# Optimization experiments

Hardware: AMD Instinct MI355X
Metric: run time of the kernel (lower is better)

Reference implementation:

```python
import jax, jax.numpy as jnp
import numpy as np

N = 100000          # total atoms in batch
M = 12              # max_num_neighbors
A = 64              # num_atom_features
B = 41              # num_bond_features
EPS = 1e-5          # haiku BatchNorm default


def setup_inputs() -> dict:
    key = jax.random.key(0)
    ks = jax.random.split(key, 6)
    neighbor_indices = jax.random.randint(ks[0], (N, M), 0, N, dtype=jnp.int32)
    atom_features = jax.random.normal(ks[1], (N, A), dtype=jnp.float32)
    bond_features = jax.random.normal(ks[2], (N, M, B), dtype=jnp.float32)
    in_f = 2 * A + B
    stdv = 1.0 / np.sqrt(in_f)
    W = jax.random.uniform(ks[3], (in_f, 2 * A), minval=-stdv, maxval=stdv, dtype=jnp.float32)
    b = jax.random.uniform(ks[4], (2 * A,), minval=-stdv, maxval=stdv, dtype=jnp.float32)
    return {
        "neighbor_indices": neighbor_indices,
        "atom_features": atom_features,
        "bond_features": bond_features,
        "W": W,
        "b": b,
        "bn1_scale": jnp.ones((2 * A,), jnp.float32),
        "bn1_offset": jnp.zeros((2 * A,), jnp.float32),
        "bn2_scale": jnp.ones((A,), jnp.float32),
        "bn2_offset": jnp.zeros((A,), jnp.float32),
    }


def _batchnorm(x, scale, offset):
    # training-mode batch norm over leading axis
    mean = jnp.mean(x, axis=0)
    var = jnp.var(x, axis=0)
    return (x - mean) * jax.lax.rsqrt(var + EPS) * scale + offset


def reference(neighbor_indices, atom_features, bond_features, W, b,
              bn1_scale, bn1_offset, bn2_scale, bn2_offset):
    n, m = neighbor_indices.shape
    a = atom_features.shape[1]
    # gather neighbor atom features: (N, M, A)
    nbr_feats = atom_features[neighbor_indices]
    self_feats = jnp.broadcast_to(atom_features[:, None, :], (n, m, a))
    total = jnp.concatenate([self_feats, nbr_feats, bond_features], axis=2)  # (N, M, 2A+B)
    gated = total @ W + b                                                    # (N, M, 2A)
    gated = _batchnorm(gated.reshape(-1, 2 * a), bn1_scale, bn1_offset).reshape(n, m, 2 * a)
    nbr_filter, nbr_core = jnp.split(gated, 2, axis=2)
    summed = jnp.sum(jax.nn.sigmoid(nbr_filter) * jax.nn.softplus(nbr_core), axis=1)  # (N, A)
    summed = _batchnorm(summed, bn2_scale, bn2_offset)
    return jax.nn.softplus(atom_features + summed)
```

## Files before the change

kernel.cpp:

```cpp
#include <hip/hip_runtime.h>

#define NATOM 100000
#define MNBR  12
#define RTOT  1200000
#define KF    169
#define NT    25000
#define NBP   1024
#define EPS   1e-5f

typedef short  bf16x8 __attribute__((ext_vector_type(8)));
typedef float  f32x4  __attribute__((ext_vector_type(4)));
typedef unsigned short us8 __attribute__((ext_vector_type(8)));

static __device__ __forceinline__ unsigned short f2bf(float x) {
    unsigned int u = __builtin_bit_cast(unsigned int, x);
    u = u + 0x7FFFu + ((u >> 16) & 1u);
    return (unsigned short)(u >> 16);
}
static __device__ __forceinline__ float softplus_f(float x) {
    return fmaxf(x, 0.f) + __logf(1.f + __expf(-fabsf(x)));
}
__device__ __forceinline__ void gload16(const void* g, void* l) {
    __builtin_amdgcn_global_load_lds((const __attribute__((address_space(1))) void*)g,
                                     (__attribute__((address_space(3))) void*)l, 16, 0, 0);
}
#define FENCE() asm volatile("" ::: "memory")

__global__ __launch_bounds__(256) void k0conv(const float* __restrict__ bond,
                                              const float* __restrict__ atom,
                                              const float* __restrict__ W,
                                              unsigned short* __restrict__ bondbf,
                                              unsigned short* __restrict__ atombf,
                                              unsigned short* __restrict__ Wbf) {
    int b = blockIdx.x;
    if (b < 28125) {
        int j0 = (b * 256 + (int)threadIdx.x) * 8;
        int r  = j0 / 48;
        int q  = j0 - r * 48;
        us8 o;
        #pragma unroll
        for (int e = 0; e < 8; ++e) {
            int c = q + e;
            float v = (c < 41) ? bond[(size_t)r * 41 + c] : 0.f;
            o[e] = f2bf(v);
        }
        *(us8*)(bondbf + j0) = o;
    } else if (b < 31250) {
        int i8 = ((b - 28125) * 256 + (int)threadIdx.x) * 8;
        float4 v0 = *(const float4*)(atom + i8);
        float4 v1 = *(const float4*)(atom + i8 + 4);
        us8 o;
        o[0]=f2bf(v0.x); o[1]=f2bf(v0.y); o[2]=f2bf(v0.z); o[3]=f2bf(v0.w);
        o[4]=f2bf(v1.x); o[5]=f2bf(v1.y); o[6]=f2bf(v1.z); o[7]=f2bf(v1.w);
        *(us8*)(atombf + i8) = o;
    } else {
        int i = (b - 31250) * 256 + (int)threadIdx.x;
        if (i < 128 * 192) {
            int c = i / 192, k = i - c * 192;
            Wbf[i] = (k < KF) ? f2bf(W[k * 128 + c]) : (unsigned short)0;
        }
    }
}

__global__ __launch_bounds__(256) void k_stats(const float* __restrict__ part,
                                               const float* __restrict__ scale,
                                               const float* __restrict__ offset,
                                               float* __restrict__ stats,
                                               int ncols, float invR) {
    int c = blockIdx.x, t = threadIdx.x;
    const float* ps = part + (size_t)c * NBP;
    const float* pq = part + (size_t)(ncols + c) * NBP;
    float s = 0.f, q = 0.f;
    for (int i = t; i < NBP; i += 256) { s += ps[i]; q += pq[i]; }
    __shared__ float rs[256], rq[256];
    rs[t] = s; rq[t] = q;
    __syncthreads();
    for (int o = 128; o > 0; o >>= 1) {
        if (t < o) { rs[t] += rs[t + o]; rq[t] += rq[t + o]; }
        __syncthreads();
    }
    if (t == 0) {
        float mean = rs[0] * invR;
        float var  = rq[0] * invR - mean * mean;
        float g = scale[c] * rsqrtf(var + EPS);
        stats[c] = g;
        stats[ncols + c] = offset[c] - mean * g;
    }
}

template<int PASS>
__global__ __launch_bounds__(256, 4) void kpass(const int* __restrict__ idx,
                                                const unsigned short* __restrict__ atombf,
                                                const unsigned short* __restrict__ bondbf,
                                                const unsigned short* __restrict__ Wbf,
                                                const float* __restrict__ stats1,
                                                float* __restrict__ part,
                                                float* __restrict__ summed) {
    __shared__ unsigned short AB[2][8704];
    __shared__ float sm[256];

    const int tid = threadIdx.x;
    const int wv  = tid >> 6;
    const int ln  = tid & 63;
    const int l15 = ln & 15;
    const int kq  = ln >> 4;
    const int blk = blockIdx.x;
    const int cf  = wv * 16 + l15;

    bf16x8 wfr[2][6];
    #pragma unroll
    for (int h = 0; h < 2; ++h) {
        int col = cf + h * 64;
        #pragma unroll
        for (int kc = 0; kc < 6; ++kc)
            wfr[h][kc] = *(const bf16x8*)((const char*)Wbf + col * 384 + kc * 64 + kq * 16);
    }
    float gf=0.f, hf=0.f, gc=0.f, hc=0.f;
    if (PASS == 2) {
        gf = stats1[cf];       hf = stats1[128 + cf];
        gc = stats1[64 + cf];  hc = stats1[192 + cf];
        sm[tid] = 0.f;
    }
    float s0 = 0.f, q0 = 0.f, s1 = 0.f, q1 = 0.f;

    int idxreg[4];
    auto PREFIDX = [&](int t) {
        #pragma unroll
        for (int j = 0; j < 4; ++j) {
            int i = wv * 4 + j;
            if (i >= 6 && i < 12) {
                int o = (i - 6) * 1024 + ln * 16;
                idxreg[j] = idx[t * 48 + (o >> 7)];
            }
        }
    };
    auto STAGE = [&](int t, int bsel) {
        unsigned short* buf = &AB[bsel][0];
        #pragma unroll
        for (int j = 0; j < 4; ++j) {
            int i = wv * 4 + j;
            if (i < 6) {
                int o  = i * 1024 + ln * 16;
                int os = o ^ (((o >> 7) & 7) << 4);
                int row = o >> 7;
                int n = (t * 48 + row) / 12;
                gload16(atombf + n * 64 + ((os & 127) >> 1), buf + (o >> 1));
            } else if (i < 12) {
                int o  = (i - 6) * 1024 + ln * 16;
                int os = o ^ (((o >> 7) & 7) << 4);
                int n = idxreg[j];
                gload16(atombf + n * 64 + ((os & 127) >> 1), buf + 3072 + (o >> 1));
            } else {
                int o = (i - 12) * 1024 + ln * 16;
                gload16(bondbf + (size_t)t * 2304 + (o >> 1), buf + 6144 + (o >> 1));
            }
        }
        if (wv == 0) {
            int o = 4 * 1024 + ln * 16;
            gload16(bondbf + (size_t)t * 2304 + (o >> 1), buf + 6144 + (o >> 1));
        }
    };

    int t0 = blk;
    PREFIDX(t0);
    asm volatile("s_waitcnt vmcnt(0)" ::: "memory");
    STAGE(t0, 0);
    if (t0 + NBP < NT) PREFIDX(t0 + NBP);

    int b = 0;
    for (int t = t0; t < NT; t += NBP) {
        bool hn = (t + NBP) < NT;
        if (PASS == 2) asm volatile("s_waitcnt lgkmcnt(0)" ::: "memory");
        __builtin_amdgcn_s_barrier();
        FENCE();
        if (hn) STAGE(t + NBP, b ^ 1);
        if (hn) {
            if (wv == 0) asm volatile("s_waitcnt vmcnt(5)" ::: "memory");
            else         asm volatile("s_waitcnt vmcnt(4)" ::: "memory");
        } else {
            asm volatile("s_waitcnt vmcnt(0)" ::: "memory");
        }
        __builtin_amdgcn_s_barrier();
        FENCE();

        const unsigned short* buf = &AB[b][0];
        f32x4 z = {0.f, 0.f, 0.f, 0.f};
        f32x4 acc[2][3];
        #pragma unroll
        for (int s = 0; s < 3; ++s) { acc[0][s] = z; acc[1][s] = z; }

        #pragma unroll
        for (int sub = 0; sub < 3; ++sub) {
            int row = sub * 16 + l15;
            #pragma unroll
            for (int kc = 0; kc < 6; ++kc) {
                const char* p;
                if (kc < 2)
                    p = (const char*)buf + ((row * 128 + kc * 64 + kq * 16) ^ ((row & 7) << 4));
                else if (kc < 4)
                    p = (const char*)(buf + 3072) + ((row * 128 + (kc - 2) * 64 + kq * 16) ^ ((row & 7) << 4));
                else
                    p = (const char*)(buf + 6144) + (row * 96 + (kc - 4) * 64 + kq * 16);
                bf16x8 a = *(const bf16x8*)p;
                acc[0][sub] = __builtin_amdgcn_mfma_f32_16x16x32_bf16(a, wfr[0][kc], acc[0][sub], 0, 0, 0);
                acc[1][sub] = __builtin_amdgcn_mfma_f32_16x16x32_bf16(a, wfr[1][kc], acc[1][sub], 0, 0, 0);
            }
        }

        if (PASS == 1) {
            #pragma unroll
            for (int sub = 0; sub < 3; ++sub)
                #pragma unroll
                for (int rg = 0; rg < 4; ++rg) {
                    float v0 = acc[0][sub][rg]; s0 += v0; q0 = fmaf(v0, v0, q0);
                    float v1 = acc[1][sub][rg]; s1 += v1; q1 = fmaf(v1, v1, q1);
                }
        } else {
            #pragma unroll
            for (int sub = 0; sub < 3; ++sub) {
                float ps = 0.f;
                #pragma unroll
                for (int rg = 0; rg < 4; ++rg) {
                    float yf = fmaf(acc[0][sub][rg], gf, hf);
                    float yc = fmaf(acc[1][sub][rg], gc, hc);
                    float sig = __builtin_amdgcn_rcpf(1.f + __expf(-yf));
                    ps = fmaf(sig, softplus_f(yc), ps);
                }
                int a = (sub * 16 + kq * 4) / 12;
                atomicAdd(&sm[a * 64 + cf], ps);
            }
            asm volatile("s_waitcnt lgkmcnt(0)" ::: "memory");
            __builtin_amdgcn_s_barrier();
            FENCE();
            float v = sm[tid];
            sm[tid] = 0.f;
            summed[(size_t)t * 256 + tid] = v;
            s0 += v; q0 = fmaf(v, v, q0);
        }
        b ^= 1;
        if (t + 2 * NBP < NT) PREFIDX(t + 2 * NBP);
    }

    if (PASS == 1) {
        s0 += __shfl_xor(s0, 16); s0 += __shfl_xor(s0, 32);
        q0 += __shfl_xor(q0, 16); q0 += __shfl_xor(q0, 32);
        s1 += __shfl_xor(s1, 16); s1 += __shfl_xor(s1, 32);
        q1 += __shfl_xor(q1, 16); q1 += __shfl_xor(q1, 32);
        if (ln < 16) {
            part[(size_t)cf * NBP + blk]          = s0;
            part[(size_t)(128 + cf) * NBP + blk]  = q0;
            part[(size_t)(64 + cf) * NBP + blk]   = s1;
            part[(size_t)(192 + cf) * NBP + blk]  = q1;
        }
    } else {
        __syncthreads();
        float* fs = (float*)&AB[0][0];
        fs[tid] = s0; fs[256 + tid] = q0;
        __syncthreads();
        if (tid < 64) {
            float S = fs[tid] + fs[tid + 64] + fs[tid + 128] + fs[tid + 192];
            float Q = fs[256 + tid] + fs[256 + tid + 64] + fs[256 + tid + 128] + fs[256 + tid + 192];
            part[(size_t)tid * NBP + blk]        = S;
            part[(size_t)(64 + tid) * NBP + blk] = Q;
        }
    }
}

__global__ __launch_bounds__(256) void k5_out(const float* __restrict__ atom,
                                              const float* __restrict__ summed,
                                              const float* __restrict__ stats2,
                                              float* __restrict__ out) {
    int i4 = blockIdx.x * 256 + threadIdx.x;
    int base = i4 * 4;
    int c = base & 63;
    float4 av = *(const float4*)(atom + base);
    float4 sv = *(const float4*)(summed + base);
    float4 ov;
    ov.x = softplus_f(av.x + stats2[c + 0] * sv.x + stats2[64 + c + 0]);
    ov.y = softplus_f(av.y + stats2[c + 1] * sv.y + stats2[64 + c + 1]);
    ov.z = softplus_f(av.z + stats2[c + 2] * sv.z + stats2[64 + c + 2]);
    ov.w = softplus_f(av.w + stats2[c + 3] * sv.w + stats2[64 + c + 3]);
    *(float4*)(out + base) = ov;
}

extern "C" void kernel_launch(void* const* d_in, const int* in_sizes, int n_in,
                              void* d_out, int out_size, void* d_ws, size_t ws_size,
                              hipStream_t stream) {
    const int*   idx  = (const int*)  d_in[0];
    const float* atom = (const float*)d_in[1];
    const float* bond = (const float*)d_in[2];
    const float* W    = (const float*)d_in[3];
    const float* bn1s = (const float*)d_in[5];
    const float* bn1o = (const float*)d_in[6];
    const float* bn2s = (const float*)d_in[7];
    const float* bn2o = (const float*)d_in[8];
    float* out = (float*)d_out;

    char* ws = (char*)d_ws;
    size_t off = 0;
    unsigned short* atombf = (unsigned short*)(ws + off); off += 12800000;
    unsigned short* bondbf = (unsigned short*)(ws + off); off += 115201024;
    unsigned short* Wbf    = (unsigned short*)(ws + off); off += 49152;
    float* part1  = (float*)(ws + off); off += 256 * NBP * 4;
    float* stats1 = (float*)(ws + off); off += 1024;
    float* part2  = (float*)(ws + off); off += 128 * NBP * 4;
    float* stats2 = (float*)(ws + off); off += 512;
    float* summed = (float*)(ws + off); off += 25600000;

    k0conv <<<31346, 256, 0, stream>>>(bond, atom, W, bondbf, atombf, Wbf);
    kpass<1><<<NBP, 256, 0, stream>>>(idx, atombf, bondbf, Wbf, stats1, part1, summed);
    k_stats<<<128, 256, 0, stream>>>(part1, bn1s, bn1o, stats1, 128, 1.f / (float)RTOT);
    kpass<2><<<NBP, 256, 0, stream>>>(idx, atombf, bondbf, Wbf, stats1, part2, summed);
    k_stats<<<64, 256, 0, stream>>>(part2, bn2s, bn2o, stats2, 64, 1.f / (float)NATOM);
    k5_out <<<6250, 256, 0, stream>>>(atom, summed, stats2, out);
}
```

Measured before the change: 584.7 us.

## Precompute self-atom projection and restructure passes into 512-thread blocks

Adds a kernel that computes each atom's self-feature contribution (atom @ W_self) once per atom rather than once per neighbor row. The main passes then drop the self K-chunks from the MFMA loop and add the staged precomputed value instead. Blocks double to 512 threads covering 96 rows per tile. Neighbor indices are now prefetched through LDS via global_load_lds, and the bond conversion kernel is rewritten to stage through shared memory for coalesced reads. This cuts MFMA work by about a third, at the cost of an extra N×128 fp32 buffer that must be written and then re-read in both passes, and a simpler single-stage wait (vmcnt(0)) that may reduce overlap.

```diff
diff --git a/kernel.cpp b/kernel.cpp
--- a/kernel.cpp
+++ b/kernel.cpp
@@ -4,9 +4,12 @@
 #define MNBR  12
 #define RTOT  1200000
 #define KF    169
-#define NT    25000
-#define NBP   1024
+#define NT    12500
+#define NBP   512
+#define IDXB  4800000
 #define EPS   1e-5f
+
+#define LBSZ  26752
 
 typedef short  bf16x8 __attribute__((ext_vector_type(8)));
 typedef float  f32x4  __attribute__((ext_vector_type(4)));
@@ -33,20 +36,25 @@
                                               unsigned short* __restrict__ atombf,
                                               unsigned short* __restrict__ Wbf) {
     int b = blockIdx.x;
-    if (b < 28125) {
-        int j0 = (b * 256 + (int)threadIdx.x) * 8;
-        int r  = j0 / 48;
-        int q  = j0 - r * 48;
-        us8 o;
-        #pragma unroll
-        for (int e = 0; e < 8; ++e) {
-            int c = q + e;
-            float v = (c < 41) ? bond[(size_t)r * 41 + c] : 0.f;
-            o[e] = f2bf(v);
-        }
-        *(us8*)(bondbf + j0) = o;
-    } else if (b < 31250) {
-        int i8 = ((b - 28125) * 256 + (int)threadIdx.x) * 8;
+    if (b < 9375) {
+        __shared__ float Lf[5248];
+        const float* src = bond + (size_t)b * 5248;
+        for (int i = threadIdx.x; i < 5248; i += 256) Lf[i] = src[i];
+        __syncthreads();
+        unsigned short* dst = bondbf + (size_t)b * 6144;
+        for (int cc = threadIdx.x; cc < 768; cc += 256) {
+            int row = cc / 6;
+            int cs  = (cc - row * 6) * 8;
+            us8 o;
+            #pragma unroll
+            for (int e = 0; e < 8; ++e) {
+                int col = cs + e;
+                o[e] = (col < 41) ? f2bf(Lf[row * 41 + col]) : (unsigned short)0;
+            }
+            *(us8*)(dst + cc * 8) = o;
+        }
+    } else if (b < 9375 + 3125) {
+        int i8 = ((b - 9375) * 256 + (int)threadIdx.x) * 8;
         float4 v0 = *(const float4*)(atom + i8);
         float4 v1 = *(const float4*)(atom + i8 + 4);
         us8 o;
@@ -54,11 +62,34 @@
         o[4]=f2bf(v1.x); o[5]=f2bf(v1.y); o[6]=f2bf(v1.z); o[7]=f2bf(v1.w);
         *(us8*)(atombf + i8) = o;
     } else {
-        int i = (b - 31250) * 256 + (int)threadIdx.x;
+        int i = (b - 12500) * 256 + (int)threadIdx.x;
         if (i < 128 * 192) {
             int c = i / 192, k = i - c * 192;
             Wbf[i] = (k < KF) ? f2bf(W[k * 128 + c]) : (unsigned short)0;
         }
+    }
+}
+
+__global__ __launch_bounds__(256) void k0spre(const unsigned short* __restrict__ atombf,
+                                              const unsigned short* __restrict__ Wbf,
+                                              float* __restrict__ Spre) {
+    int blk = blockIdx.x;
+    int tid = threadIdx.x, wv = tid >> 6, ln = tid & 63, l15 = ln & 15, kq = ln >> 4;
+    int rowa = blk * 64 + wv * 16 + l15;
+    int rla  = rowa < NATOM ? rowa : NATOM - 1;
+    bf16x8 af0 = *(const bf16x8*)(atombf + (size_t)rla * 64 + kq * 8);
+    bf16x8 af1 = *(const bf16x8*)(atombf + (size_t)rla * 64 + 32 + kq * 8);
+    int rowo = blk * 64 + wv * 16 + kq * 4;
+    #pragma unroll
+    for (int ct = 0; ct < 8; ++ct) {
+        f32x4 a = {0.f, 0.f, 0.f, 0.f};
+        bf16x8 w0 = *(const bf16x8*)((const char*)Wbf + (ct*16+l15)*384 + 0  + kq*16);
+        bf16x8 w1 = *(const bf16x8*)((const char*)Wbf + (ct*16+l15)*384 + 64 + kq*16);
+        a = __builtin_amdgcn_mfma_f32_16x16x32_bf16(af0, w0, a, 0, 0, 0);
+        a = __builtin_amdgcn_mfma_f32_16x16x32_bf16(af1, w1, a, 0, 0, 0);
+        #pragma unroll
+        for (int rg = 0; rg < 4; ++rg)
+            if (rowo + rg < NATOM) Spre[(size_t)(rowo + rg) * 128 + ct * 16 + l15] = a[rg];
     }
 }
 
@@ -68,10 +99,12 @@
                                                float* __restrict__ stats,
                                                int ncols, float invR) {
     int c = blockIdx.x, t = threadIdx.x;
-    const float* ps = part + (size_t)c * NBP;
-    const float* pq = part + (size_t)(ncols + c) * NBP;
+    int stride = 2 * ncols;
     float s = 0.f, q = 0.f;
-    for (int i = t; i < NBP; i += 256) { s += ps[i]; q += pq[i]; }
+    for (int i = t; i < NBP; i += 256) {
+        s += part[(size_t)i * stride + c];
+        q += part[(size_t)i * stride + ncols + c];
+    }
     __shared__ float rs[256], rq[256];
     rs[t] = s; rq[t] = q;
     __syncthreads();
@@ -89,101 +122,105 @@
 }
 
 template<int PASS>
-__global__ __launch_bounds__(256, 4) void kpass(const int* __restrict__ idx,
+__global__ __launch_bounds__(512, 4) void kpass(const int* __restrict__ idxg,
                                                 const unsigned short* __restrict__ atombf,
                                                 const unsigned short* __restrict__ bondbf,
                                                 const unsigned short* __restrict__ Wbf,
+                                                const float* __restrict__ Spre,
                                                 const float* __restrict__ stats1,
                                                 float* __restrict__ part,
                                                 float* __restrict__ summed) {
-    __shared__ unsigned short AB[2][8704];
-    __shared__ float sm[256];
+    __shared__ __align__(16) unsigned char LB[2][LBSZ];
+    __shared__ float sm[512];
 
     const int tid = threadIdx.x;
     const int wv  = tid >> 6;
     const int ln  = tid & 63;
     const int l15 = ln & 15;
     const int kq  = ln >> 4;
+    const int rh  = wv >> 2;
+    const int cg  = wv & 3;
+    const int cf  = cg * 16 + l15;
     const int blk = blockIdx.x;
-    const int cf  = wv * 16 + l15;
-
-    bf16x8 wfr[2][6];
+
+    const char* atomc = (const char*)atombf;
+    const char* bondc = (const char*)bondbf;
+    const char* sprec = (const char*)Spre;
+    const char* idxc  = (const char*)idxg;
+
+    sm[tid] = 0.f;
+    if (tid < 16) {
+        f32x4 z4 = {0.f, 0.f, 0.f, 0.f};
+        *(f32x4*)(&LB[tid >> 3][21504 + (tid & 7) * 16]) = z4;
+    }
+
+    bf16x8 wfr[2][4];
     #pragma unroll
     for (int h = 0; h < 2; ++h) {
         int col = cf + h * 64;
         #pragma unroll
-        for (int kc = 0; kc < 6; ++kc)
-            wfr[h][kc] = *(const bf16x8*)((const char*)Wbf + col * 384 + kc * 64 + kq * 16);
-    }
-    float gf=0.f, hf=0.f, gc=0.f, hc=0.f;
+        for (int j = 0; j < 4; ++j)
+            wfr[h][j] = *(const bf16x8*)((const char*)Wbf + col * 384 + (j + 2) * 64 + kq * 16);
+    }
+    float gf = 0.f, hf = 0.f, gc = 0.f, hc = 0.f;
     if (PASS == 2) {
         gf = stats1[cf];       hf = stats1[128 + cf];
         gc = stats1[64 + cf];  hc = stats1[192 + cf];
-        sm[tid] = 0.f;
     }
     float s0 = 0.f, q0 = 0.f, s1 = 0.f, q1 = 0.f;
 
-    int idxreg[4];
-    auto PREFIDX = [&](int t) {
-        #pragma unroll
-        for (int j = 0; j < 4; ++j) {
-            int i = wv * 4 + j;
-            if (i >= 6 && i < 12) {
-                int o = (i - 6) * 1024 + ln * 16;
-                idxreg[j] = idx[t * 48 + (o >> 7)];
-            }
+    const int nbrlane = (((ln & 7) ^ (ln >> 3)) << 4);
+    const int r0row   = 8 * wv + (ln >> 3);
+
+    auto STAGE = [&](int u, int bb, int iv0, int iv1) {
+        unsigned char* buf = &LB[bb][0];
+        if (wv < 4) {
+            gload16(atomc + (size_t)iv0 * 128 + nbrlane, buf + wv * 1024 + ln * 16);
+            gload16(atomc + (size_t)iv1 * 128 + nbrlane, buf + (wv + 8) * 1024 + ln * 16);
+            gload16(bondc + (size_t)u * 9216 + (wv + 4) * 1024 + ln * 16,
+                    buf + 12288 + (wv + 4) * 1024 + ln * 16);
+            if (wv == 0)
+                gload16(sprec + (size_t)u * 4096 + 3 * 1024 + ln * 16,
+                        buf + 21632 + 3 * 1024 + ln * 16);
+            if (wv == 1 && (u + NBP) < NT) {
+                int B = min((u + NBP) * 384, IDXB - 1024);
+                gload16(idxc + B + ln * 16, buf + 25728 + ln * 16);
+            }
+        } else {
+            int w4 = wv - 4;
+            gload16(atomc + (size_t)iv0 * 128 + nbrlane, buf + wv * 1024 + ln * 16);
+            gload16(bondc + (size_t)u * 9216 + w4 * 1024 + ln * 16,
+                    buf + 12288 + w4 * 1024 + ln * 16);
+            if (wv == 4)
+                gload16(bondc + (size_t)u * 9216 + 8 * 1024 + ln * 16,
+                        buf + 12288 + 8 * 1024 + ln * 16);
+            else
+                gload16(sprec + (size_t)u * 4096 + (w4 - 1) * 1024 + ln * 16,
+                        buf + 21632 + (w4 - 1) * 1024 + ln * 16);
         }
     };
-    auto STAGE = [&](int t, int bsel) {
-        unsigned short* buf = &AB[bsel][0];
-        #pragma unroll
-        for (int j = 0; j < 4; ++j) {
-            int i = wv * 4 + j;
-            if (i < 6) {
-                int o  = i * 1024 + ln * 16;
-                int os = o ^ (((o >> 7) & 7) << 4);
-                int row = o >> 7;
-                int n = (t * 48 + row) / 12;
-                gload16(atombf + n * 64 + ((os & 127) >> 1), buf + (o >> 1));
-            } else if (i < 12) {
-                int o  = (i - 6) * 1024 + ln * 16;
-                int os = o ^ (((o >> 7) & 7) << 4);
-                int n = idxreg[j];
-                gload16(atombf + n * 64 + ((os & 127) >> 1), buf + 3072 + (o >> 1));
-            } else {
-                int o = (i - 12) * 1024 + ln * 16;
-                gload16(bondbf + (size_t)t * 2304 + (o >> 1), buf + 6144 + (o >> 1));
-            }
-        }
-        if (wv == 0) {
-            int o = 4 * 1024 + ln * 16;
-            gload16(bondbf + (size_t)t * 2304 + (o >> 1), buf + 6144 + (o >> 1));
-        }
-    };
-
-    int t0 = blk;
-    PREFIDX(t0);
-    asm volatile("s_waitcnt vmcnt(0)" ::: "memory");
-    STAGE(t0, 0);
-    if (t0 + NBP < NT) PREFIDX(t0 + NBP);
+
+    const int u0 = blk;
+    {
+        int iv0 = idxg[u0 * 96 + r0row];
+        int iv1 = (wv < 4) ? idxg[u0 * 96 + 64 + r0row] : 0;
+        STAGE(u0, 0, iv0, iv1);
+    }
 
     int b = 0;
-    for (int t = t0; t < NT; t += NBP) {
-        bool hn = (t + NBP) < NT;
-        if (PASS == 2) asm volatile("s_waitcnt lgkmcnt(0)" ::: "memory");
+    for (int u = u0; u < NT; u += NBP) {
+        asm volatile("s_waitcnt vmcnt(0) lgkmcnt(0)" ::: "memory");
         __builtin_amdgcn_s_barrier();
         FENCE();
-        if (hn) STAGE(t + NBP, b ^ 1);
-        if (hn) {
-            if (wv == 0) asm volatile("s_waitcnt vmcnt(5)" ::: "memory");
-            else         asm volatile("s_waitcnt vmcnt(4)" ::: "memory");
-        } else {
-            asm volatile("s_waitcnt vmcnt(0)" ::: "memory");
-        }
-        __builtin_amdgcn_s_barrier();
-        FENCE();
-
-        const unsigned short* buf = &AB[b][0];
+        if (u + NBP < NT) {
+            int delta4 = max(0, (u + NBP) * 384 - (IDXB - 1024)) >> 2;
+            const int* idxs = (const int*)(&LB[b][25728]);
+            int iv0 = idxs[delta4 + r0row];
+            int iv1 = (wv < 4) ? idxs[delta4 + 64 + r0row] : 0;
+            STAGE(u + NBP, b ^ 1, iv0, iv1);
+        }
+
+        const unsigned char* buf = &LB[b][0];
         f32x4 z = {0.f, 0.f, 0.f, 0.f};
         f32x4 acc[2][3];
         #pragma unroll
@@ -191,54 +228,60 @@
 
         #pragma unroll
         for (int sub = 0; sub < 3; ++sub) {
-            int row = sub * 16 + l15;
-            #pragma unroll
-            for (int kc = 0; kc < 6; ++kc) {
-                const char* p;
-                if (kc < 2)
-                    p = (const char*)buf + ((row * 128 + kc * 64 + kq * 16) ^ ((row & 7) << 4));
-                else if (kc < 4)
-                    p = (const char*)(buf + 3072) + ((row * 128 + (kc - 2) * 64 + kq * 16) ^ ((row & 7) << 4));
+            int rowa = rh * 48 + sub * 16 + l15;
+            #pragma unroll
+            for (int j = 0; j < 4; ++j) {
+                const unsigned char* p;
+                if (j < 2)
+                    p = buf + ((rowa * 128 + j * 64 + kq * 16) ^ ((rowa & 7) << 4));
                 else
-                    p = (const char*)(buf + 6144) + (row * 96 + (kc - 4) * 64 + kq * 16);
+                    p = buf + 12288 + rowa * 96 + (j - 2) * 64 + kq * 16;
                 bf16x8 a = *(const bf16x8*)p;
-                acc[0][sub] = __builtin_amdgcn_mfma_f32_16x16x32_bf16(a, wfr[0][kc], acc[0][sub], 0, 0, 0);
-                acc[1][sub] = __builtin_amdgcn_mfma_f32_16x16x32_bf16(a, wfr[1][kc], acc[1][sub], 0, 0, 0);
-            }
-        }
-
+                acc[0][sub] = __builtin_amdgcn_mfma_f32_16x16x32_bf16(a, wfr[0][j], acc[0][sub], 0, 0, 0);
+                acc[1][sub] = __builtin_amdgcn_mfma_f32_16x16x32_bf16(a, wfr[1][j], acc[1][sub], 0, 0, 0);
+            }
+        }
+
+        const float* spref = (const float*)(&LB[b][21632]);
         if (PASS == 1) {
             #pragma unroll
-            for (int sub = 0; sub < 3; ++sub)
+            for (int sub = 0; sub < 3; ++sub) {
+                int aL = (rh * 48 + sub * 16 + kq * 4) / 12;
+                float sp0 = spref[aL * 128 + cf];
+                float sp1 = spref[aL * 128 + 64 + cf];
                 #pragma unroll
                 for (int rg = 0; rg < 4; ++rg) {
-                    float v0 = acc[0][sub][rg]; s0 += v0; q0 = fmaf(v0, v0, q0);
-                    float v1 = acc[1][sub][rg]; s1 += v1; q1 = fmaf(v1, v1, q1);
+                    float v0 = acc[0][sub][rg] + sp0; s0 += v0; q0 = fmaf(v0, v0, q0);
+                    float v1 = acc[1][sub][rg] + sp1; s1 += v1; q1 = fmaf(v1, v1, q1);
                 }
+            }
         } else {
             #pragma unroll
             for (int sub = 0; sub < 3; ++sub) {
+                int aL = (rh * 48 + sub * 16 + kq * 4) / 12;
+                float sp0 = spref[aL * 128 + cf];
+                float sp1 = spref[aL * 128 + 64 + cf];
+                float hf2 = fmaf(sp0, gf, hf);
+                float hc2 = fmaf(sp1, gc, hc);
                 float ps = 0.f;
                 #pragma unroll
                 for (int rg = 0; rg < 4; ++rg) {
-                    float yf = fmaf(acc[0][sub][rg], gf, hf);
-                    float yc = fmaf(acc[1][sub][rg], gc, hc);
+                    float yf = fmaf(acc[0][sub][rg], gf, hf2);
+                    float yc = fmaf(acc[1][sub][rg], gc, hc2);
                     float sig = __builtin_amdgcn_rcpf(1.f + __expf(-yf));
                     ps = fmaf(sig, softplus_f(yc), ps);
                 }
-                int a = (sub * 16 + kq * 4) / 12;
-                atomicAdd(&sm[a * 64 + cf], ps);
+                atomicAdd(&sm[aL * 64 + cf], ps);
             }
             asm volatile("s_waitcnt lgkmcnt(0)" ::: "memory");
             __builtin_amdgcn_s_barrier();
             FENCE();
             float v = sm[tid];
             sm[tid] = 0.f;
-            summed[(size_t)t * 256 + tid] = v;
+            summed[(size_t)u * 512 + tid] = v;
             s0 += v; q0 = fmaf(v, v, q0);
         }
         b ^= 1;
-        if (t + 2 * NBP < NT) PREFIDX(t + 2 * NBP);
     }
 
     if (PASS == 1) {
@@ -247,21 +290,22 @@
         s1 += __shfl_xor(s1, 16); s1 += __shfl_xor(s1, 32);
         q1 += __shfl_xor(q1, 16); q1 += __shfl_xor(q1, 32);
         if (ln < 16) {
-            part[(size_t)cf * NBP + blk]          = s0;
-            part[(size_t)(128 + cf) * NBP + blk]  = q0;
-            part[(size_t)(64 + cf) * NBP + blk]   = s1;
-            part[(size_t)(192 + cf) * NBP + blk]  = q1;
-        }
+            atomicAdd(&sm[cf], s0);        atomicAdd(&sm[128 + cf], q0);
+            atomicAdd(&sm[64 + cf], s1);   atomicAdd(&sm[192 + cf], q1);
+        }
+        __syncthreads();
+        if (tid < 256) part[(size_t)blk * 256 + tid] = sm[tid];
     } else {
         __syncthreads();
-        float* fs = (float*)&AB[0][0];
-        fs[tid] = s0; fs[256 + tid] = q0;
+        float* fs = (float*)(&LB[0][0]);
+        fs[tid] = s0; fs[512 + tid] = q0;
         __syncthreads();
         if (tid < 64) {
-            float S = fs[tid] + fs[tid + 64] + fs[tid + 128] + fs[tid + 192];
-            float Q = fs[256 + tid] + fs[256 + tid + 64] + fs[256 + tid + 128] + fs[256 + tid + 192];
-            part[(size_t)tid * NBP + blk]        = S;
-            part[(size_t)(64 + tid) * NBP + blk] = Q;
+            float S = 0.f, Q = 0.f;
+            #pragma unroll
+            for (int g = 0; g < 8; ++g) { S += fs[tid + 64 * g]; Q += fs[512 + tid + 64 * g]; }
+            part[(size_t)blk * 128 + tid]      = S;
+            part[(size_t)blk * 128 + 64 + tid] = Q;
         }
     }
 }
@@ -301,16 +345,18 @@
     unsigned short* atombf = (unsigned short*)(ws + off); off += 12800000;
     unsigned short* bondbf = (unsigned short*)(ws + off); off += 115201024;
     unsigned short* Wbf    = (unsigned short*)(ws + off); off += 49152;
-    float* part1  = (float*)(ws + off); off += 256 * NBP * 4;
+    float* Spre   = (float*)(ws + off); off += (size_t)NATOM * 128 * 4;
+    float* part1  = (float*)(ws + off); off += (size_t)NBP * 256 * 4;
     float* stats1 = (float*)(ws + off); off += 1024;
-    float* part2  = (float*)(ws + off); off += 128 * NBP * 4;
+    float* part2  = (float*)(ws + off); off += (size_t)NBP * 128 * 4;
     float* stats2 = (float*)(ws + off); off += 512;
-    float* summed = (float*)(ws + off); off += 25600000;
-
-    k0conv <<<31346, 256, 0, stream>>>(bond, atom, W, bondbf, atombf, Wbf);
-    kpass<1><<<NBP, 256, 0, stream>>>(idx, atombf, bondbf, Wbf, stats1, part1, summed);
+    float* summed = (float*)(ws + off); off += (size_t)NATOM * 64 * 4;
+
+    k0conv <<<12596, 256, 0, stream>>>(bond, atom, W, bondbf, atombf, Wbf);
+    k0spre <<<1563, 256, 0, stream>>>(atombf, Wbf, Spre);
+    kpass<1><<<NBP, 512, 0, stream>>>(idx, atombf, bondbf, Wbf, Spre, stats1, part1, summed);
     k_stats<<<128, 256, 0, stream>>>(part1, bn1s, bn1o, stats1, 128, 1.f / (float)RTOT);
-    kpass<2><<<NBP, 256, 0, stream>>>(idx, atombf, bondbf, Wbf, stats1, part2, summed);
+    kpass<2><<<NBP, 512, 0, stream>>>(idx, atombf, bondbf, Wbf, Spre, stats1, part2, summed);
     k_stats<<<64, 256, 0, stream>>>(part2, bn2s, bn2o, stats2, 64, 1.f / (float)NATOM);
-    k5_out <<<6250, 256, 0, stream>>>(atom, summed, stats2, out);
-}
+    k5_out <<<(NATOM * 64 / 4 + 255) / 256, 256, 0, stream>>>(atom, summed, stats2, out);
+}
```

After: 549.3 us. 6.1% less time.
